# Kernel optimization log

Hardware: AMD Instinct MI355X
Metric: run time of the kernel (lower is better)

## Reference

```python
import jax, jax.numpy as jnp
import numpy as np

B, N, EMBED = 4, 2048, 512
H, EXPAND = 8, 3
D1 = (EXPAND * EMBED) // H * H   # 1536
HD = D1 // H                     # 192
RPE = int(min(EMBED / 8, 32))    # 32 (overridden in __init__)
EPS = 1e-8


def _srms(x, d):
    # SimpleRMSNorm: x / (||x||_2 * d^-0.5 + eps); no learnable params
    nrm = jnp.linalg.norm(x, axis=-1, keepdims=True)
    return x / (nrm * (d ** -0.5) + EPS)


def setup_inputs() -> dict:
    key = jax.random.key(0)
    ks = iter(jax.random.split(key, 32))
    w = lambda shape, s=0.02: jax.random.normal(next(ks), shape, dtype=jnp.float32) * s
    return {
        "xyz": jax.random.normal(next(ks), (B, N, 3), dtype=jnp.float32),
        "x": jax.random.normal(next(ks), (B, N, EMBED), dtype=jnp.float32),
        "u_w": w((EMBED, D1)), "u_b": w((D1,)),
        "v_w": w((EMBED, D1)), "v_b": w((D1,)),
        "o_w": w((D1, EMBED)), "o_b": w((EMBED,)),
        "rpe_pos_w": w((1, RPE)), "rpe_pos_b": w((RPE,)),
        "rpe_lyr_w": w((3, RPE, RPE)), "rpe_lyr_b": w((3, RPE)),
        "rpe_out_w": w((RPE, H * HD)), "rpe_out_b": w((H * HD,)),
        "glu1_w": w((EMBED, D1)), "glu1_b": w((D1,)),
        "glu2_w": w((EMBED, D1)), "glu2_b": w((D1,)),
        "glu3_w": w((D1, EMBED)), "glu3_b": w((EMBED,)),
    }


def _rpe_mlp(idx, pw, pb, lw, lb, ow, ob):
    # idx: [m, 1] positions -> [H, m, HD] Toeplitz coefficients
    h = jax.nn.relu(idx @ pw + pb)
    for i in range(lw.shape[0]):  # fixed small layer count (3), non-residual
        h = jax.nn.relu(_srms(h, RPE)) @ lw[i] + lb[i]
    o = jax.nn.relu(_srms(h, RPE)) @ ow + ob  # [m, H*HD]
    return o.reshape(-1, H, HD).transpose(1, 0, 2)


def reference(xyz, x, u_w, u_b, v_w, v_b, o_w, o_b,
              rpe_pos_w, rpe_pos_b, rpe_lyr_w, rpe_lyr_b,
              rpe_out_w, rpe_out_b,
              glu1_w, glu1_b, glu2_w, glu2_b, glu3_w, glu3_b):
    b, n, _ = x.shape
    shortcut = x
    # NOTE: original builds SimpleRMSNorm(d1) but applies it to embed_dim
    # features, so the divisor uses d1^-0.5. Preserved faithfully.
    xn = _srms(x, D1)
    u = jax.nn.silu(xn @ u_w + u_b)                      # b n d1
    v = jax.nn.silu(xn @ v_w + v_b)
    v = v.reshape(b, n, H, HD).transpose(0, 2, 1, 3)     # b h n d
    # --- Tno non-causal (par_type=1, no decay, act_type='none') ---
    rpe = lambda idx: _rpe_mlp(idx, rpe_pos_w, rpe_pos_b, rpe_lyr_w,
                               rpe_lyr_b, rpe_out_w, rpe_out_b)
    zero = rpe(jnp.zeros((1, 1), dtype=x.dtype))                     # h 1 d
    pos = rpe(jnp.arange(1, n, dtype=x.dtype)[:, None])              # h n-1 d
    neg = rpe(-jnp.arange(n - 1, 0, -1, dtype=x.dtype)[:, None])     # h n-1 d
    a = jnp.concatenate([zero, pos, zero, neg], axis=1)              # h 2n d
    # Toeplitz matmul as length-2n circular convolution via FFT
    yf = jnp.fft.rfft(v, 2 * n, axis=-2)
    af = jnp.fft.rfft(a, 2 * n, axis=-2)[None]
    t = jnp.fft.irfft(yf * af, 2 * n, axis=-2)[:, :, :n, :]          # b h n d
    t = t.transpose(0, 2, 1, 3).reshape(b, n, D1)
    out = (u * t) @ o_w + o_b
    x2 = out + shortcut
    # GLU (fina_act='None', dropout=0)
    g = (jax.nn.silu(x2 @ glu1_w + glu1_b) * (x2 @ glu2_w + glu2_b)) @ glu3_w + glu3_b
    return (g, out)
```

## Files before the change

### kernel.cpp

```cpp
#include <hip/hip_runtime.h>
#include <math.h>

#define NSEQ 2048
#define NFFT 4096
#define D1C  1536
#define EMBC 512
#define BATCH 4

typedef __fp16 f16;
typedef __fp16 f16x8 __attribute__((ext_vector_type(8)));
typedef __fp16 f16x4 __attribute__((ext_vector_type(4)));
typedef float  f32x4 __attribute__((ext_vector_type(4)));
typedef unsigned int u32;

__device__ __forceinline__ float silu_f(float y) { return y / (1.f + expf(-y)); }

__global__ __launch_bounds__(256) void scale_kernel(const float* __restrict__ x,
                                                    float* __restrict__ scale) {
    int row  = blockIdx.x * 4 + (threadIdx.x >> 6);
    int lane = threadIdx.x & 63;
    const float* xr = x + (size_t)row * EMBC;
    float ss = 0.f;
#pragma unroll
    for (int k = 0; k < EMBC / 64; ++k) { float v = xr[lane + k * 64]; ss += v * v; }
#pragma unroll
    for (int off = 32; off >= 1; off >>= 1) ss += __shfl_xor(ss, off);
    if (lane == 0) scale[row] = 1.f / (sqrtf(ss) * 0.02551551815399144f + 1e-8f);
}

__global__ __launch_bounds__(256) void convert_xn_kernel(
    const float* __restrict__ x, const float* __restrict__ scale,
    f16* __restrict__ xh, f16* __restrict__ xl) {
    size_t i = ((size_t)blockIdx.x * 256 + threadIdx.x) * 4;
    float4 v = *reinterpret_cast<const float4*>(x + i);
    float s = scale[i >> 9];
    f16x4 h, l;
    const float* vv = (const float*)&v;
#pragma unroll
    for (int j = 0; j < 4; ++j) {
        float val = vv[j] * s;
        f16 hh = (f16)val;
        h[j] = hh; l[j] = (f16)(val - (float)hh);
    }
    *reinterpret_cast<f16x4*>(xh + i) = h;
    *reinterpret_cast<f16x4*>(xl + i) = l;
}

__global__ __launch_bounds__(256) void convert_x2_kernel(
    const float* __restrict__ a, const float* __restrict__ b,
    f16* __restrict__ xh, f16* __restrict__ xl) {
    size_t i = ((size_t)blockIdx.x * 256 + threadIdx.x) * 4;
    float4 va = *reinterpret_cast<const float4*>(a + i);
    float4 vb = *reinterpret_cast<const float4*>(b + i);
    const float* pa = (const float*)&va;
    const float* pb = (const float*)&vb;
    f16x4 h, l;
#pragma unroll
    for (int j = 0; j < 4; ++j) {
        float val = pa[j] + pb[j];
        f16 hh = (f16)val;
        h[j] = hh; l[j] = (f16)(val - (float)hh);
    }
    *reinterpret_cast<f16x4*>(xh + i) = h;
    *reinterpret_cast<f16x4*>(xl + i) = l;
}

__global__ __launch_bounds__(256) void wtrans_kernel(const float* __restrict__ W,
        f16* __restrict__ Th, int Kd, int Nd) {
    __shared__ float t[32][33];
    int tx = threadIdx.x & 31, ty = threadIdx.x >> 5;
    int n0 = blockIdx.x * 32, k0 = blockIdx.y * 32;
#pragma unroll
    for (int yy = ty; yy < 32; yy += 8)
        t[yy][tx] = W[(size_t)(k0 + yy) * Nd + n0 + tx];
    __syncthreads();
#pragma unroll
    for (int yy = ty; yy < 32; yy += 8) {
        float v = t[tx][yy];
        Th[(size_t)(n0 + yy) * Kd + k0 + tx] = (f16)v;
    }
}

__global__ __launch_bounds__(256) void convert_p_kernel(
    const float* __restrict__ u, const float* __restrict__ vt,
    f16* __restrict__ ph, f16* __restrict__ pl) {
    __shared__ float t[32][33];
    int b = blockIdx.z, n0 = blockIdx.x * 32, c0 = blockIdx.y * 32;
    int tx = threadIdx.x & 31, ty = threadIdx.x >> 5;
#pragma unroll
    for (int yy = ty; yy < 32; yy += 8)
        t[yy][tx] = vt[(((size_t)(b * D1C + c0 + yy)) << 11) + n0 + tx];
    __syncthreads();
#pragma unroll
    for (int yy = ty; yy < 32; yy += 8) {
        int row = b * NSEQ + n0 + yy;
        size_t idx = (size_t)row * D1C + c0 + tx;
        float val = u[idx] * t[tx][yy];
        f16 h = (f16)val;
        ph[idx] = h; pl[idx] = (f16)(val - (float)h);
    }
}

__global__ __launch_bounds__(256) void rpe_kernel(
    const float* __restrict__ pw, const float* __restrict__ pb,
    const float* __restrict__ lw, const float* __restrict__ lb,
    const float* __restrict__ ow, const float* __restrict__ ob,
    float* __restrict__ a_r) {
    __shared__ float hs[64][33];
    int tid = threadIdx.x;
    int s0  = blockIdx.x * 64;
    if (tid < 64) {
        int s = s0 + tid;
        float p = (s == 0 || s == 2048) ? 0.f : (s < 2048 ? (float)s : (float)(s - 4096));
        float h[32];
#pragma unroll
        for (int k = 0; k < 32; ++k) h[k] = fmaxf(p * pw[k] + pb[k], 0.f);
        for (int L = 0; L < 3; ++L) {
            float ss = 0.f;
#pragma unroll
            for (int k = 0; k < 32; ++k) ss += h[k] * h[k];
            float sc = 1.f / (sqrtf(ss) * 0.1767766952966369f + 1e-8f);
            float g[32];
#pragma unroll
            for (int k = 0; k < 32; ++k) g[k] = fmaxf(h[k] * sc, 0.f);
#pragma unroll
            for (int j = 0; j < 32; ++j) {
                float acc = lb[L * 32 + j];
#pragma unroll
                for (int k = 0; k < 32; ++k) acc += g[k] * lw[(L * 32 + k) * 32 + j];
                h[j] = acc;
            }
        }
        float ss = 0.f;
#pragma unroll
        for (int k = 0; k < 32; ++k) ss += h[k] * h[k];
        float sc = 1.f / (sqrtf(ss) * 0.1767766952966369f + 1e-8f);
#pragma unroll
        for (int k = 0; k < 32; ++k) hs[tid][k] = fmaxf(h[k] * sc, 0.f);
    }
    __syncthreads();
    for (int cc = 0; cc < 6; ++cc) {
        int col = tid + cc * 256;
        float wcol[32];
#pragma unroll
        for (int k = 0; k < 32; ++k) wcol[k] = ow[k * D1C + col];
        float bb = ob[col];
        float* outp = a_r + ((size_t)col << 12) + s0;
        for (int r = 0; r < 64; ++r) {
            float acc = bb;
#pragma unroll
            for (int k = 0; k < 32; ++k) acc += hs[r][k] * wcol[k];
            outp[r] = acc;
        }
    }
}

#define PHI(i) ((i) + ((i) >> 5))
#define FPAD 4224

__device__ __forceinline__ void fft_fwd(float* re, float* im, int tid, bool halfInput) {
    for (int m = 1024; m >= 1; m >>= 2) {
        __syncthreads();
        float c0 = -(float)M_PI * 0.5f / (float)m;
        for (int p = tid; p < 1024; p += 256) {
            int j  = p & (m - 1);
            int i0 = ((p - j) << 2) + j;
            int i1 = i0 + m, i2 = i1 + m, i3 = i2 + m;
            float x0r = re[PHI(i0)], x0i = im[PHI(i0)];
            float x1r = re[PHI(i1)], x1i = im[PHI(i1)];
            float x2r, x2i, x3r, x3i;
            if (halfInput && m == 1024) { x2r = 0.f; x2i = 0.f; x3r = 0.f; x3i = 0.f; }
            else { x2r = re[PHI(i2)]; x2i = im[PHI(i2)];
                   x3r = re[PHI(i3)]; x3i = im[PHI(i3)]; }
            float ar = x0r + x2r, ai = x0i + x2i;
            float br = x0r - x2r, bi = x0i - x2i;
            float cr = x1r + x3r, ci = x1i + x3i;
            float dr = x1r - x3r, di = x1i - x3i;
            re[PHI(i0)] = ar + cr; im[PHI(i0)] = ai + ci;
            float s1, c1; __sincosf(c0 * (float)j, &s1, &c1);
            float c2 = c1 * c1 - s1 * s1, s2 = 2.f * c1 * s1;
            float c3 = c2 * c1 - s2 * s1, s3 = s2 * c1 + c2 * s1;
            float t1r = br + di, t1i = bi - dr;
            re[PHI(i1)] = t1r * c1 - t1i * s1; im[PHI(i1)] = t1r * s1 + t1i * c1;
            float t2r = ar - cr, t2i = ai - ci;
            re[PHI(i2)] = t2r * c2 - t2i * s2; im[PHI(i2)] = t2r * s2 + t2i * c2;
            float t3r = br - di, t3i = bi + dr;
            re[PHI(i3)] = t3r * c3 - t3i * s3; im[PHI(i3)] = t3r * s3 + t3i * c3;
        }
    }
    __syncthreads();
}

__device__ __forceinline__ void fft_inv(float* re, float* im, int tid) {
    for (int m = 1; m <= 1024; m <<= 2) {
        __syncthreads();
        float c0 = (float)M_PI * 0.5f / (float)m;
        for (int p = tid; p < 1024; p += 256) {
            int j  = p & (m - 1);
            int i0 = ((p - j) << 2) + j;
            int i1 = i0 + m, i2 = i1 + m, i3 = i2 + m;
            float y0r = re[PHI(i0)], y0i = im[PHI(i0)];
            float y1r = re[PHI(i1)], y1i = im[PHI(i1)];
            float y2r = re[PHI(i2)], y2i = im[PHI(i2)];
            float y3r = re[PHI(i3)], y3i = im[PHI(i3)];
            float s1, c1; __sincosf(c0 * (float)j, &s1, &c1);
            float c2 = c1 * c1 - s1 * s1, s2 = 2.f * c1 * s1;
            float c3 = c2 * c1 - s2 * s1, s3 = s2 * c1 + c2 * s1;
            float p1r = y1r * c1 - y1i * s1, p1i = y1r * s1 + y1i * c1;
            float p2r = y2r * c2 - y2i * s2, p2i = y2r * s2 + y2i * c2;
            float p3r = y3r * c3 - y3i * s3, p3i = y3r * s3 + y3i * c3;
            float a2r = y0r + p2r, a2i = y0i + p2i;
            float g2r = y0r - p2r, g2i = y0i - p2i;
            float b2r = p1r + p3r, b2i = p1i + p3i;
            float er  = p3r - p1r, ei  = p3i - p1i;
            float d2r = ei, d2i = -er;
            re[PHI(i0)] = a2r + b2r; im[PHI(i0)] = a2i + b2i;
            re[PHI(i1)] = g2r + d2r; im[PHI(i1)] = g2i + d2i;
            re[PHI(i2)] = a2r - b2r; im[PHI(i2)] = a2i - b2i;
            re[PHI(i3)] = g2r - d2r; im[PHI(i3)] = g2i - d2i;
        }
    }
    __syncthreads();
}

__global__ __launch_bounds__(256) void fft_a_kernel(const float* __restrict__ a_r,
                                                    float2* __restrict__ af) {
    __shared__ float re[FPAD];
    __shared__ float im[FPAD];
    int tid = threadIdx.x;
    const float* row = a_r + ((size_t)blockIdx.x << 12);
    float2* orow     = af  + ((size_t)blockIdx.x << 12);
    for (int k = tid; k < NFFT; k += 256) { re[PHI(k)] = row[k]; im[PHI(k)] = 0.f; }
    fft_fwd(re, im, tid, false);
    for (int k = tid; k < NFFT; k += 256) orow[k] = make_float2(re[PHI(k)], im[PHI(k)]);
}

__global__ __launch_bounds__(256) void conv_kernel(float* __restrict__ vt,
                                                   const float2* __restrict__ af) {
    __shared__ float re[FPAD];
    __shared__ float im[FPAD];
    int tid = threadIdx.x;
    int pr  = blockIdx.x / D1C;
    int col = blockIdx.x % D1C;
    float* v0 = vt + ((size_t)((2 * pr)     * D1C + col) << 11);
    float* v1 = vt + ((size_t)((2 * pr + 1) * D1C + col) << 11);
    const float2* arow = af + ((size_t)col << 12);
    for (int k = tid; k < 2048; k += 256) { re[PHI(k)] = v0[k]; im[PHI(k)] = v1[k]; }
    fft_fwd(re, im, tid, true);
    const float inv = 1.0f / 4096.0f;
    for (int k = tid; k < NFFT; k += 256) {
        int q = PHI(k);
        float zr = re[q], zi = im[q];
        float2 w = arow[k];
        re[q] = (zr * w.x - zi * w.y) * inv;
        im[q] = (zr * w.y + zi * w.x) * inv;
    }
    fft_inv(re, im, tid);
    for (int k = tid; k < 2048; k += 256) { v0[k] = re[PHI(k)]; v1[k] = im[PHI(k)]; }
}

enum { EP_SILU_F32, EP_SILU_VT, EP_PLAIN, EP_GLU2 };

template <int BM, int K, int EPI>
__global__ __launch_bounds__(256, (BM == 128 ? 3 : 4)) void mgemm(
    const f16* __restrict__ Ah, const f16* __restrict__ Al,
    const f16* __restrict__ Bh,
    const float* __restrict__ bias, const float* __restrict__ E0,
    float* __restrict__ OutF, f16* __restrict__ OutH, f16* __restrict__ OutL,
    int Ncols) {
    constexpr int SB   = BM * 128 + 8192;
    constexpr int MREP = BM / 32;
    constexpr int LOGB = (BM == 128 ? 7 : 6);
    constexpr int CA   = BM / 64;
    __shared__ __align__(16) char smem[2 * SB];

    const int tid  = threadIdx.x;
    const int w    = tid >> 6, lane = tid & 63;
    const int wr   = w >> 1, wc = w & 1;
    const int l15  = lane & 15, kc = lane >> 4;

    const int NBY = Ncols >> 7;
    const int nwg = gridDim.x;
    int flat = blockIdx.x;
    int q8 = nwg >> 3, r8 = nwg & 7;
    int xcd = flat & 7, pos = flat >> 3;
    int wg = (xcd < r8 ? xcd * (q8 + 1) : r8 * (q8 + 1) + (xcd - r8) * q8) + pos;
    const int row0 = (wg / NBY) * BM;
    const int col0 = (wg % NBY) * 128;

    f32x4 acc[MREP][4] = {};

    auto stage = [&](int buf, int kt) {
        const int k0 = kt * 32;
        const int bb = buf * SB;
#pragma unroll
        for (int l = 0; l < CA; ++l) {
            int ci = tid + l * 256;
            int r = ci & (BM - 1), kk = ci >> LOGB;
            const f16* ga = Ah + (size_t)(row0 + r) * K + k0 + kk * 8;
            const f16* gb = Al + (size_t)(row0 + r) * K + k0 + kk * 8;
            __builtin_amdgcn_global_load_lds((const __attribute__((address_space(1))) u32*)ga,
                (__attribute__((address_space(3))) u32*)(smem + bb + ci * 16), 16, 0, 0);
            __builtin_amdgcn_global_load_lds((const __attribute__((address_space(1))) u32*)gb,
                (__attribute__((address_space(3))) u32*)(smem + bb + BM * 64 + ci * 16), 16, 0, 0);
        }
#pragma unroll
        for (int l = 0; l < 2; ++l) {
            int ci = tid + l * 256;
            int c = ci & 127, kk = ci >> 7;
            const f16* gc = Bh + (size_t)(col0 + c) * K + k0 + kk * 8;
            __builtin_amdgcn_global_load_lds((const __attribute__((address_space(1))) u32*)gc,
                (__attribute__((address_space(3))) u32*)(smem + bb + BM * 128 + ci * 16), 16, 0, 0);
        }
    };

    auto compute = [&](int buf) {
        const char* base = smem + buf * SB;
        f16x8 a_h[MREP], a_l[MREP], b_h[4];
#pragma unroll
        for (int m = 0; m < MREP; ++m) {
            int r = wr * (BM / 2) + m * 16 + l15;
            a_h[m] = *(const f16x8*)(base + (kc * BM + r) * 16);
            a_l[m] = *(const f16x8*)(base + BM * 64 + (kc * BM + r) * 16);
        }
#pragma unroll
        for (int n = 0; n < 4; ++n) {
            int c = wc * 64 + n * 16 + l15;
            b_h[n] = *(const f16x8*)(base + BM * 128 + (kc * 128 + c) * 16);
        }
#pragma unroll
        for (int m = 0; m < MREP; ++m)
#pragma unroll
            for (int n = 0; n < 4; ++n) {
                acc[m][n] = __builtin_amdgcn_mfma_f32_16x16x32_f16(a_h[m], b_h[n], acc[m][n], 0, 0, 0);
                acc[m][n] = __builtin_amdgcn_mfma_f32_16x16x32_f16(a_l[m], b_h[n], acc[m][n], 0, 0, 0);
            }
    };

    constexpr int NT = K / 32;
    stage(0, 0);
    __syncthreads();
    int cur = 0;
    for (int t = 0; t < NT; ++t) {
        if (t + 1 < NT) stage(cur ^ 1, t + 1);
        compute(cur);
        __syncthreads();
        cur ^= 1;
    }

    const int WRB = wr * (BM / 2);
    if constexpr (EPI == EP_SILU_VT) {
        float* patch = (float*)(smem + w * 5376);
#pragma unroll
        for (int m = 0; m < MREP; ++m) {
            __syncthreads();
#pragma unroll
            for (int n = 0; n < 4; ++n)
#pragma unroll
                for (int r = 0; r < 4; ++r)
                    patch[(n * 16 + l15) * 20 + kc * 4 + r] = acc[m][n][r];
            __syncthreads();
#pragma unroll
            for (int t = 0; t < 4; ++t) {
                int qi = lane + t * 64;
                int col_ = qi >> 2, rq = qi & 3;
                float4 y = *(const float4*)&patch[col_ * 20 + rq * 4];
                int col = col0 + wc * 64 + col_;
                float bb = bias[col];
                y.x = silu_f(y.x + bb); y.y = silu_f(y.y + bb);
                y.z = silu_f(y.z + bb); y.w = silu_f(y.w + bb);
                int b = row0 >> 11;
                int seq = (row0 & 2047) + WRB + m * 16 + rq * 4;
                *(float4*)&OutF[(((size_t)(b * D1C + col)) << 11) + seq] = y;
            }
        }
    } else {
        float* patch = (float*)(smem + w * 4352);
#pragma unroll
        for (int m = 0; m < MREP; ++m) {
            __syncthreads();
#pragma unroll
            for (int n = 0; n < 4; ++n)
#pragma unroll
                for (int r = 0; r < 4; ++r)
                    patch[(kc * 4 + r) * 68 + n * 16 + l15] = acc[m][n][r];
            __syncthreads();
#pragma unroll
            for (int t = 0; t < 4; ++t) {
                int qi = lane + t * 64;
                int row_ = qi >> 4, q = qi & 15;
                float4 y = *(const float4*)&patch[row_ * 68 + q * 4];
                int row = row0 + WRB + m * 16 + row_;
                int col = col0 + wc * 64 + q * 4;
                float4 bb = *(const float4*)&bias[col];
                y.x += bb.x; y.y += bb.y; y.z += bb.z; y.w += bb.w;
                size_t idx = (size_t)row * Ncols + col;
                if constexpr (EPI == EP_SILU_F32) {
                    y.x = silu_f(y.x); y.y = silu_f(y.y);
                    y.z = silu_f(y.z); y.w = silu_f(y.w);
                    *(float4*)&OutF[idx] = y;
                } else if constexpr (EPI == EP_PLAIN) {
                    *(float4*)&OutF[idx] = y;
                } else {
                    float4 e = *(const float4*)&E0[idx];
                    float z0 = e.x * y.x, z1 = e.y * y.y, z2 = e.z * y.z, z3 = e.w * y.w;
                    f16x4 h, l;
                    h[0] = (f16)z0; l[0] = (f16)(z0 - (float)h[0]);
                    h[1] = (f16)z1; l[1] = (f16)(z1 - (float)h[1]);
                    h[2] = (f16)z2; l[2] = (f16)(z2 - (float)h[2]);
                    h[3] = (f16)z3; l[3] = (f16)(z3 - (float)h[3]);
                    *(f16x4*)&OutH[idx] = h;
                    *(f16x4*)&OutL[idx] = l;
                }
            }
        }
    }
}

extern "C" void kernel_launch(void* const* d_in, const int* in_sizes, int n_in,
                              void* d_out, int out_size, void* d_ws, size_t ws_size,
                              hipStream_t stream) {
    const float* x   = (const float*)d_in[1];
    const float* u_w = (const float*)d_in[2];
    const float* u_b = (const float*)d_in[3];
    const float* v_w = (const float*)d_in[4];
    const float* v_b = (const float*)d_in[5];
    const float* o_w = (const float*)d_in[6];
    const float* o_b = (const float*)d_in[7];
    const float* rpw = (const float*)d_in[8];
    const float* rpb = (const float*)d_in[9];
    const float* rlw = (const float*)d_in[10];
    const float* rlb = (const float*)d_in[11];
    const float* row_w = (const float*)d_in[12];
    const float* rob = (const float*)d_in[13];
    const float* g1w = (const float*)d_in[14];
    const float* g1b = (const float*)d_in[15];
    const float* g2w = (const float*)d_in[16];
    const float* g2b = (const float*)d_in[17];
    const float* g3w = (const float*)d_in[18];
    const float* g3b = (const float*)d_in[19];

    char* wsb = (char*)d_ws;
    float* scale = (float*)wsb;
    char* R1 = wsb + (1 << 16);
    char* R2 = R1 + 50331648;
    char* R3 = R2 + 50331648;
    char* R4 = R3 + 50331648;
    char* R5 = R4 + 16777216;

    float2* af   = (float2*)R1;
    f16*    ph   = (f16*)R1;
    f16*    pl   = (f16*)(R1 + 25165824);
    float*  vt   = (float*)R2;
    float*  tmp1 = (float*)R2;
    float*  a_r  = (float*)R3;
    float*  u    = (float*)R3;
    f16*    zh   = (f16*)R3;
    f16*    zl   = (f16*)(R3 + 25165824);
    f16*    xnh  = (f16*)R4;
    f16*    xnl  = (f16*)(R4 + 8388608);
    f16*    x2h  = xnh;
    f16*    x2l  = xnl;

    auto wTh = [&](int i) { return (f16*)(R5 + (size_t)i * 1572864); };

    float* g_out   = (float*)d_out;
    float* out_out = g_out + (size_t)BATCH * NSEQ * EMBC;

    scale_kernel<<<2048, 256, 0, stream>>>(x, scale);
    convert_xn_kernel<<<4096, 256, 0, stream>>>(x, scale, xnh, xnl);
    wtrans_kernel<<<dim3(48, 16), 256, 0, stream>>>(u_w, wTh(0), 512, 1536);
    wtrans_kernel<<<dim3(48, 16), 256, 0, stream>>>(v_w, wTh(1), 512, 1536);
    wtrans_kernel<<<dim3(16, 48), 256, 0, stream>>>(o_w, wTh(2), 1536, 512);
    wtrans_kernel<<<dim3(48, 16), 256, 0, stream>>>(g1w, wTh(3), 512, 1536);
    wtrans_kernel<<<dim3(48, 16), 256, 0, stream>>>(g2w, wTh(4), 512, 1536);
    wtrans_kernel<<<dim3(16, 48), 256, 0, stream>>>(g3w, wTh(5), 1536, 512);
    rpe_kernel<<<64, 256, 0, stream>>>(rpw, rpb, rlw, rlb, row_w, rob, a_r);
    fft_a_kernel<<<1536, 256, 0, stream>>>(a_r, af);

    mgemm<128, 512, EP_SILU_F32><<<768, 256, 0, stream>>>(
        xnh, xnl, wTh(0), u_b, nullptr, u, nullptr, nullptr, 1536);
    mgemm<128, 512, EP_SILU_VT><<<768, 256, 0, stream>>>(
        xnh, xnl, wTh(1), v_b, nullptr, vt, nullptr, nullptr, 1536);

    conv_kernel<<<3072, 256, 0, stream>>>(vt, af);
    convert_p_kernel<<<dim3(64, 48, 4), 256, 0, stream>>>(u, vt, ph, pl);

    mgemm<64, 1536, EP_PLAIN><<<512, 256, 0, stream>>>(
        ph, pl, wTh(2), o_b, nullptr, out_out, nullptr, nullptr, 512);

    convert_x2_kernel<<<4096, 256, 0, stream>>>(out_out, x, x2h, x2l);
    mgemm<128, 512, EP_SILU_F32><<<768, 256, 0, stream>>>(
        x2h, x2l, wTh(3), g1b, nullptr, tmp1, nullptr, nullptr, 1536);
    mgemm<128, 512, EP_GLU2><<<768, 256, 0, stream>>>(
        x2h, x2l, wTh(4), g2b, tmp1, nullptr, zh, zl, 1536);
    mgemm<64, 1536, EP_PLAIN><<<512, 256, 0, stream>>>(
        zh, zl, wTh(5), g3b, nullptr, g_out, nullptr, nullptr, 512);
}
```

Baseline: 672.9 us.

## Replace radix-4 shared-memory FFT with register radix-16 three-pass FFT

```diff
diff --git a/kernel.cpp b/kernel.cpp
--- a/kernel.cpp
+++ b/kernel.cpp
@@ -155,108 +155,225 @@
     }
 }
 
-#define PHI(i) ((i) + ((i) >> 5))
-#define FPAD 4224
-
-__device__ __forceinline__ void fft_fwd(float* re, float* im, int tid, bool halfInput) {
-    for (int m = 1024; m >= 1; m >>= 2) {
-        __syncthreads();
-        float c0 = -(float)M_PI * 0.5f / (float)m;
-        for (int p = tid; p < 1024; p += 256) {
-            int j  = p & (m - 1);
-            int i0 = ((p - j) << 2) + j;
-            int i1 = i0 + m, i2 = i1 + m, i3 = i2 + m;
-            float x0r = re[PHI(i0)], x0i = im[PHI(i0)];
-            float x1r = re[PHI(i1)], x1i = im[PHI(i1)];
-            float x2r, x2i, x3r, x3i;
-            if (halfInput && m == 1024) { x2r = 0.f; x2i = 0.f; x3r = 0.f; x3i = 0.f; }
-            else { x2r = re[PHI(i2)]; x2i = im[PHI(i2)];
-                   x3r = re[PHI(i3)]; x3i = im[PHI(i3)]; }
-            float ar = x0r + x2r, ai = x0i + x2i;
-            float br = x0r - x2r, bi = x0i - x2i;
-            float cr = x1r + x3r, ci = x1i + x3i;
-            float dr = x1r - x3r, di = x1i - x3i;
-            re[PHI(i0)] = ar + cr; im[PHI(i0)] = ai + ci;
-            float s1, c1; __sincosf(c0 * (float)j, &s1, &c1);
-            float c2 = c1 * c1 - s1 * s1, s2 = 2.f * c1 * s1;
-            float c3 = c2 * c1 - s2 * s1, s3 = s2 * c1 + c2 * s1;
-            float t1r = br + di, t1i = bi - dr;
-            re[PHI(i1)] = t1r * c1 - t1i * s1; im[PHI(i1)] = t1r * s1 + t1i * c1;
-            float t2r = ar - cr, t2i = ai - ci;
-            re[PHI(i2)] = t2r * c2 - t2i * s2; im[PHI(i2)] = t2r * s2 + t2i * c2;
-            float t3r = br - di, t3i = bi + dr;
-            re[PHI(i3)] = t3r * c3 - t3i * s3; im[PHI(i3)] = t3r * s3 + t3i * c3;
-        }
-    }
-    __syncthreads();
-}
-
-__device__ __forceinline__ void fft_inv(float* re, float* im, int tid) {
-    for (int m = 1; m <= 1024; m <<= 2) {
-        __syncthreads();
-        float c0 = (float)M_PI * 0.5f / (float)m;
-        for (int p = tid; p < 1024; p += 256) {
-            int j  = p & (m - 1);
-            int i0 = ((p - j) << 2) + j;
-            int i1 = i0 + m, i2 = i1 + m, i3 = i2 + m;
-            float y0r = re[PHI(i0)], y0i = im[PHI(i0)];
-            float y1r = re[PHI(i1)], y1i = im[PHI(i1)];
-            float y2r = re[PHI(i2)], y2i = im[PHI(i2)];
-            float y3r = re[PHI(i3)], y3i = im[PHI(i3)];
-            float s1, c1; __sincosf(c0 * (float)j, &s1, &c1);
-            float c2 = c1 * c1 - s1 * s1, s2 = 2.f * c1 * s1;
-            float c3 = c2 * c1 - s2 * s1, s3 = s2 * c1 + c2 * s1;
-            float p1r = y1r * c1 - y1i * s1, p1i = y1r * s1 + y1i * c1;
-            float p2r = y2r * c2 - y2i * s2, p2i = y2r * s2 + y2i * c2;
-            float p3r = y3r * c3 - y3i * s3, p3i = y3r * s3 + y3i * c3;
-            float a2r = y0r + p2r, a2i = y0i + p2i;
-            float g2r = y0r - p2r, g2i = y0i - p2i;
-            float b2r = p1r + p3r, b2i = p1i + p3i;
-            float er  = p3r - p1r, ei  = p3i - p1i;
-            float d2r = ei, d2i = -er;
-            re[PHI(i0)] = a2r + b2r; im[PHI(i0)] = a2i + b2i;
-            re[PHI(i1)] = g2r + d2r; im[PHI(i1)] = g2i + d2i;
-            re[PHI(i2)] = a2r - b2r; im[PHI(i2)] = a2i - b2i;
-            re[PHI(i3)] = g2r - d2r; im[PHI(i3)] = g2i - d2i;
-        }
-    }
-    __syncthreads();
-}
-
-__global__ __launch_bounds__(256) void fft_a_kernel(const float* __restrict__ a_r,
-                                                    float2* __restrict__ af) {
-    __shared__ float re[FPAD];
-    __shared__ float im[FPAD];
+#define LIDX(e) ((e) + ((((e) >> 4)) << 1))
+
+template <bool INV, bool HALF>
+__device__ __forceinline__ void dft16(const float* xr, const float* xi,
+                                      float* outr, float* outi) {
+    constexpr float C1 = 0.92387953251f, S1 = 0.38268343236f, R2 = 0.70710678119f;
+    constexpr float sg = INV ? 1.f : -1.f;
+    float tr[16], ti[16];
+#pragma unroll
+    for (int n0 = 0; n0 < 4; ++n0) {
+        float ar = xr[n0], ai = xi[n0];
+        float br = xr[n0 + 4], bi = xi[n0 + 4];
+        float j0r, j0i, j1r, j1i, j2r, j2i, j3r, j3i;
+        if constexpr (HALF) {
+            j0r = ar + br; j0i = ai + bi;
+            j2r = ar - br; j2i = ai - bi;
+            if constexpr (!INV) { j1r = ar + bi; j1i = ai - br; j3r = ar - bi; j3i = ai + br; }
+            else                { j1r = ar - bi; j1i = ai + br; j3r = ar + bi; j3i = ai - br; }
+        } else {
+            float cr = xr[n0 + 8],  ci = xi[n0 + 8];
+            float dr = xr[n0 + 12], di = xi[n0 + 12];
+            float t0r = ar + cr, t0i = ai + ci;
+            float t1r = ar - cr, t1i = ai - ci;
+            float t2r = br + dr, t2i = bi + di;
+            float t3r = br - dr, t3i = bi - di;
+            j0r = t0r + t2r; j0i = t0i + t2i;
+            j2r = t0r - t2r; j2i = t0i - t2i;
+            if constexpr (!INV) { j1r = t1r + t3i; j1i = t1i - t3r;
+                                  j3r = t1r - t3i; j3i = t1i + t3r; }
+            else                { j1r = t1r - t3i; j1i = t1i + t3r;
+                                  j3r = t1r + t3i; j3i = t1i - t3r; }
+        }
+        tr[n0] = j0r;      ti[n0] = j0i;
+        tr[n0 + 4] = j1r;  ti[n0 + 4] = j1i;
+        tr[n0 + 8] = j2r;  ti[n0 + 8] = j2i;
+        tr[n0 + 12] = j3r; ti[n0 + 12] = j3i;
+    }
+#define CMK(idx, wr_, wi_) { float _r = tr[idx], _i = ti[idx]; \
+        tr[idx] = _r * (wr_) - _i * (wi_); ti[idx] = _r * (wi_) + _i * (wr_); }
+    CMK(5,  C1, sg * S1)  CMK(6,  R2, sg * R2)  CMK(7,  S1, sg * C1)
+    CMK(9,  R2, sg * R2)
+    { float _r = tr[10];
+      if constexpr (!INV) { tr[10] = ti[10];  ti[10] = -_r; }
+      else                { tr[10] = -ti[10]; ti[10] = _r;  } }
+    CMK(11, -R2, sg * R2)
+    CMK(13, S1, sg * C1)  CMK(14, -R2, sg * R2)  CMK(15, -C1, -sg * S1)
+#undef CMK
+#pragma unroll
+    for (int j = 0; j < 4; ++j) {
+        float ar = tr[4 * j],     ai = ti[4 * j];
+        float br = tr[4 * j + 1], bi = ti[4 * j + 1];
+        float cr = tr[4 * j + 2], ci = ti[4 * j + 2];
+        float dr = tr[4 * j + 3], di = ti[4 * j + 3];
+        float t0r = ar + cr, t0i = ai + ci;
+        float t1r = ar - cr, t1i = ai - ci;
+        float t2r = br + dr, t2i = bi + di;
+        float t3r = br - dr, t3i = bi - di;
+        outr[j]      = t0r + t2r; outi[j]      = t0i + t2i;
+        outr[8 + j]  = t0r - t2r; outi[8 + j]  = t0i - t2i;
+        if constexpr (!INV) {
+            outr[4 + j]  = t1r + t3i; outi[4 + j]  = t1i - t3r;
+            outr[12 + j] = t1r - t3i; outi[12 + j] = t1i + t3r;
+        } else {
+            outr[4 + j]  = t1r - t3i; outi[4 + j]  = t1i + t3r;
+            outr[12 + j] = t1r + t3i; outi[12 + j] = t1i - t3r;
+        }
+    }
+}
+
+#define CMUL_ADV(wr, wi, sr, si) { float _n = (wr)*(sr) - (wi)*(si); \
+        (wi) = (wr)*(si) + (wi)*(sr); (wr) = _n; }
+
+__global__ __launch_bounds__(256, 4) void fft_a_kernel(const float* __restrict__ a_r,
+                                                       float2* __restrict__ af) {
+    __shared__ float2 buf[4608];
     int tid = threadIdx.x;
     const float* row = a_r + ((size_t)blockIdx.x << 12);
     float2* orow     = af  + ((size_t)blockIdx.x << 12);
-    for (int k = tid; k < NFFT; k += 256) { re[PHI(k)] = row[k]; im[PHI(k)] = 0.f; }
-    fft_fwd(re, im, tid, false);
-    for (int k = tid; k < NFFT; k += 256) orow[k] = make_float2(re[PHI(k)], im[PHI(k)]);
-}
-
-__global__ __launch_bounds__(256) void conv_kernel(float* __restrict__ vt,
-                                                   const float2* __restrict__ af) {
-    __shared__ float re[FPAD];
-    __shared__ float im[FPAD];
+    float xr[16], xi[16], yr[16], yi[16];
+    float bsr, bsi, wr, wi;
+#pragma unroll
+    for (int a = 0; a < 16; ++a) { xr[a] = row[a * 256 + tid]; xi[a] = 0.f; }
+    dft16<false, false>(xr, xi, yr, yi);
+    __sincosf(-(float)M_PI / 2048.f * (float)tid, &bsi, &bsr);
+    wr = bsr; wi = bsi;
+    buf[LIDX(tid)] = make_float2(yr[0], yi[0]);
+#pragma unroll
+    for (int k0 = 1; k0 < 16; ++k0) {
+        buf[LIDX(k0 * 256 + tid)] =
+            make_float2(yr[k0] * wr - yi[k0] * wi, yr[k0] * wi + yi[k0] * wr);
+        CMUL_ADV(wr, wi, bsr, bsi);
+    }
+    __syncthreads();
+    int k0 = tid >> 4, cc = tid & 15;
+    int base2 = k0 * 256 + cc;
+#pragma unroll
+    for (int b = 0; b < 16; ++b) {
+        float2 v = buf[LIDX(base2 + b * 16)]; xr[b] = v.x; xi[b] = v.y;
+    }
+    dft16<false, false>(xr, xi, yr, yi);
+    __sincosf(-(float)M_PI / 128.f * (float)cc, &bsi, &bsr);
+    wr = bsr; wi = bsi;
+    buf[LIDX(base2)] = make_float2(yr[0], yi[0]);
+#pragma unroll
+    for (int k1 = 1; k1 < 16; ++k1) {
+        buf[LIDX(base2 + k1 * 16)] =
+            make_float2(yr[k1] * wr - yi[k1] * wi, yr[k1] * wi + yi[k1] * wr);
+        CMUL_ADV(wr, wi, bsr, bsi);
+    }
+    __syncthreads();
+    const float4* pld = (const float4*)&buf[18 * tid];
+#pragma unroll
+    for (int h = 0; h < 8; ++h) {
+        float4 q = pld[h];
+        xr[2 * h] = q.x; xi[2 * h] = q.y; xr[2 * h + 1] = q.z; xi[2 * h + 1] = q.w;
+    }
+    dft16<false, false>(xr, xi, yr, yi);
+#pragma unroll
+    for (int k2 = 0; k2 < 16; ++k2)
+        orow[k2 * 256 + tid] = make_float2(yr[k2], yi[k2]);
+}
+
+__global__ __launch_bounds__(256, 4) void conv_kernel(float* __restrict__ vt,
+                                                      const float2* __restrict__ af) {
+    __shared__ float2 buf[4608];
     int tid = threadIdx.x;
     int pr  = blockIdx.x / D1C;
     int col = blockIdx.x % D1C;
     float* v0 = vt + ((size_t)((2 * pr)     * D1C + col) << 11);
     float* v1 = vt + ((size_t)((2 * pr + 1) * D1C + col) << 11);
     const float2* arow = af + ((size_t)col << 12);
-    for (int k = tid; k < 2048; k += 256) { re[PHI(k)] = v0[k]; im[PHI(k)] = v1[k]; }
-    fft_fwd(re, im, tid, true);
+    float xr[16], xi[16], yr[16], yi[16];
+    float bsr, bsi, wr, wi;
+
+#pragma unroll
+    for (int a = 0; a < 8; ++a) { xr[a] = v0[a * 256 + tid]; xi[a] = v1[a * 256 + tid]; }
+    dft16<false, true>(xr, xi, yr, yi);
+    __sincosf(-(float)M_PI / 2048.f * (float)tid, &bsi, &bsr);
+    wr = bsr; wi = bsi;
+    buf[LIDX(tid)] = make_float2(yr[0], yi[0]);
+#pragma unroll
+    for (int k0 = 1; k0 < 16; ++k0) {
+        buf[LIDX(k0 * 256 + tid)] =
+            make_float2(yr[k0] * wr - yi[k0] * wi, yr[k0] * wi + yi[k0] * wr);
+        CMUL_ADV(wr, wi, bsr, bsi);
+    }
+    __syncthreads();
+    int k0 = tid >> 4, cc = tid & 15;
+    int base2 = k0 * 256 + cc;
+#pragma unroll
+    for (int b = 0; b < 16; ++b) {
+        float2 v = buf[LIDX(base2 + b * 16)]; xr[b] = v.x; xi[b] = v.y;
+    }
+    dft16<false, false>(xr, xi, yr, yi);
+    __sincosf(-(float)M_PI / 128.f * (float)cc, &bsi, &bsr);
+    wr = bsr; wi = bsi;
+    buf[LIDX(base2)] = make_float2(yr[0], yi[0]);
+#pragma unroll
+    for (int k1 = 1; k1 < 16; ++k1) {
+        buf[LIDX(base2 + k1 * 16)] =
+            make_float2(yr[k1] * wr - yi[k1] * wi, yr[k1] * wi + yi[k1] * wr);
+        CMUL_ADV(wr, wi, bsr, bsi);
+    }
+    __syncthreads();
+    const float4* pld = (const float4*)&buf[18 * tid];
+#pragma unroll
+    for (int h = 0; h < 8; ++h) {
+        float4 q = pld[h];
+        xr[2 * h] = q.x; xi[2 * h] = q.y; xr[2 * h + 1] = q.z; xi[2 * h + 1] = q.w;
+    }
+    dft16<false, false>(xr, xi, yr, yi);
     const float inv = 1.0f / 4096.0f;
-    for (int k = tid; k < NFFT; k += 256) {
-        int q = PHI(k);
-        float zr = re[q], zi = im[q];
-        float2 w = arow[k];
-        re[q] = (zr * w.x - zi * w.y) * inv;
-        im[q] = (zr * w.y + zi * w.x) * inv;
-    }
-    fft_inv(re, im, tid);
-    for (int k = tid; k < 2048; k += 256) { v0[k] = re[PHI(k)]; v1[k] = im[PHI(k)]; }
+#pragma unroll
+    for (int k2 = 0; k2 < 16; ++k2) {
+        float2 w = arow[k2 * 256 + tid];
+        float rr = (yr[k2] * w.x - yi[k2] * w.y) * inv;
+        float ii = (yr[k2] * w.y + yi[k2] * w.x) * inv;
+        xr[k2] = rr; xi[k2] = ii;
+    }
+    dft16<true, false>(xr, xi, yr, yi);
+    __sincosf((float)M_PI / 128.f * (float)cc, &bsi, &bsr);
+    wr = bsr; wi = bsi;
+#pragma unroll
+    for (int c = 1; c < 16; ++c) {
+        float rr = yr[c] * wr - yi[c] * wi;
+        yi[c] = yr[c] * wi + yi[c] * wr; yr[c] = rr;
+        CMUL_ADV(wr, wi, bsr, bsi);
+    }
+    float4* pst = (float4*)&buf[18 * tid];
+#pragma unroll
+    for (int h = 0; h < 8; ++h)
+        pst[h] = make_float4(yr[2 * h], yi[2 * h], yr[2 * h + 1], yi[2 * h + 1]);
+    __syncthreads();
+#pragma unroll
+    for (int k1 = 0; k1 < 16; ++k1) {
+        float2 v = buf[LIDX(base2 + k1 * 16)]; xr[k1] = v.x; xi[k1] = v.y;
+    }
+    dft16<true, false>(xr, xi, yr, yi);
+    float swr, swi;
+    __sincosf((float)M_PI / 2048.f * (float)(k0 * cc), &bsi, &bsr);
+    __sincosf((float)M_PI / 128.f * (float)k0, &swi, &swr);
+    wr = bsr; wi = bsi;
+#pragma unroll
+    for (int b = 0; b < 16; ++b) {
+        buf[LIDX(base2 + b * 16)] =
+            make_float2(yr[b] * wr - yi[b] * wi, yr[b] * wi + yi[b] * wr);
+        CMUL_ADV(wr, wi, swr, swi);
+    }
+    __syncthreads();
+#pragma unroll
+    for (int k = 0; k < 16; ++k) {
+        float2 v = buf[LIDX(k * 256 + tid)]; xr[k] = v.x; xi[k] = v.y;
+    }
+    dft16<true, false>(xr, xi, yr, yi);
+#pragma unroll
+    for (int a = 0; a < 8; ++a) {
+        v0[a * 256 + tid] = yr[a];
+        v1[a * 256 + tid] = yi[a];
+    }
 }
 
 enum { EP_SILU_F32, EP_SILU_VT, EP_PLAIN, EP_GLU2 };
```

After: 676.0 us. Within noise of the previous version (+0.5%).
